# Optimization experiments

Hardware: AMD Instinct MI355X
Metric: run time of the kernel (lower is better)

Reference implementation:

```python
import jax, jax.numpy as jnp
import numpy as np

B, IN_DIM, OUT_DIM, DEGREE = 4096, 1024, 1024, 4
LN_EPS = 1e-5


def setup_inputs() -> dict:
    key = jax.random.key(0)
    k_x, k_c = jax.random.split(key)
    x = jax.random.normal(k_x, (B, IN_DIM), dtype=jnp.float32)
    # xavier_normal_ on tensor of shape (in, out, deg+1): fan_in/fan_out from
    # torch convention: fan_in = out*(deg+1)? torch computes fan_in=size(1)*receptive,
    # for 3D tensor fan_in = shape[1]*shape[2], fan_out = shape[0]*shape[2].
    fan_in = OUT_DIM * (DEGREE + 1)
    fan_out = IN_DIM * (DEGREE + 1)
    std = float(np.sqrt(2.0 / (fan_in + fan_out)))
    cheby_coeffs = jax.random.normal(k_c, (IN_DIM, OUT_DIM, DEGREE + 1), dtype=jnp.float32) * std
    ln_weight = jnp.ones((IN_DIM,), dtype=jnp.float32)
    ln_bias = jnp.zeros((IN_DIM,), dtype=jnp.float32)
    return {"x": x, "cheby_coeffs": cheby_coeffs, "ln_weight": ln_weight, "ln_bias": ln_bias}


def _layer_norm(x, w, b):
    mu = jnp.mean(x, axis=-1, keepdims=True)
    var = jnp.mean(jnp.square(x - mu), axis=-1, keepdims=True)
    return (x - mu) * jax.lax.rsqrt(var + LN_EPS) * w + b


def reference(x, cheby_coeffs, ln_weight, ln_bias):
    h = jnp.tanh(_layer_norm(x, ln_weight, ln_bias))  # [B, I]
    # Chebyshev recurrence T0=1, T1=h, T_{n}=2h*T_{n-1}-T_{n-2}
    cheby = [jnp.ones_like(h), h]
    for _ in range(2, DEGREE + 1):
        cheby.append(2.0 * h * cheby[-1] - cheby[-2])
    stacked = jnp.stack(cheby, axis=-1)  # [B, I, D+1]
    y = jnp.einsum('bid,iod->bo', stacked, cheby_coeffs)
    return jax.nn.silu(y)
```

## Files before the change

kernel.cpp:

```cpp
#include <hip/hip_runtime.h>
#include <cstdint>
#include <cstddef>

#define BATCH 4096
#define IDIM 1024
#define ODIM 1024
#define KDIM 4096
#define KHALF 2048

typedef __attribute__((ext_vector_type(8))) short bf16x8;
typedef __attribute__((ext_vector_type(4))) float f32x4;

__device__ __forceinline__ unsigned short f2bf(float f) {
  union { float f; unsigned int u; } v; v.f = f;
  unsigned int r = (v.u + 0x7FFFu + ((v.u >> 16) & 1u)) >> 16;
  return (unsigned short)r;
}
__device__ __forceinline__ float bf2f(unsigned short u) {
  union { unsigned int u; float f; } v; v.u = ((unsigned int)u) << 16;
  return v.f;
}

__device__ __forceinline__ void load_lds16(const void* g, void* l) {
  __builtin_amdgcn_global_load_lds(
      (const __attribute__((address_space(1))) void*)g,
      (__attribute__((address_space(3))) void*)l, 16, 0, 0);
}

__device__ __forceinline__ int sidx(int p, int ii) {
  return p * 64 + ((ii + 4 * (p & 15)) & 63);
}

__global__ __launch_bounds__(256) void prep(
    const float* __restrict__ x, const float* __restrict__ lnw,
    const float* __restrict__ lnb, const float* __restrict__ C,
    unsigned short* __restrict__ A, unsigned short* __restrict__ Bt,
    float* __restrict__ biasPart) {
  __shared__ __align__(16) unsigned short sm[64 * 5 * 64];
  int bid = blockIdx.x;
  int t = threadIdx.x;

  if (bid < BATCH) {
    float* rs = (float*)sm;
    float* rq = ((float*)sm) + 4;
    const float4 v = ((const float4*)(x + (size_t)bid * IDIM))[t];
    float s  = v.x + v.y + v.z + v.w;
    float s2 = v.x * v.x + v.y * v.y + v.z * v.z + v.w * v.w;
#pragma unroll
    for (int off = 32; off > 0; off >>= 1) {
      s  += __shfl_down(s, off);
      s2 += __shfl_down(s2, off);
    }
    int lane = t & 63, wv = t >> 6;
    if (lane == 0) { rs[wv] = s; rq[wv] = s2; }
    __syncthreads();
    float S1 = rs[0] + rs[1] + rs[2] + rs[3];
    float S2 = rq[0] + rq[1] + rq[2] + rq[3];
    float mean = S1 * (1.0f / IDIM);
    float var  = S2 * (1.0f / IDIM) - mean * mean;
    float rstd = rsqrtf(var + 1e-5f);

    const float4 w4 = ((const float4*)lnw)[t];
    const float4 b4 = ((const float4*)lnb)[t];
    float xs[4]  = {v.x, v.y, v.z, v.w};
    float ws4[4] = {w4.x, w4.y, w4.z, w4.w};
    float bs4[4] = {b4.x, b4.y, b4.z, b4.w};

    unsigned short u1[4], u2[4], u3[4], u4[4];
#pragma unroll
    for (int j = 0; j < 4; j++) {
      float h  = tanhf((xs[j] - mean) * rstd * ws4[j] + bs4[j]);
      float T2 = 2.0f * h * h - 1.0f;
      float T3 = 2.0f * h * T2 - h;
      float T4 = 2.0f * h * T3 - T2;
      u1[j] = f2bf(h); u2[j] = f2bf(T2); u3[j] = f2bf(T3); u4[j] = f2bf(T4);
    }
    size_t base = (size_t)bid * KDIM;
    *(ushort4*)(A + base + 0 * IDIM + t * 4) = *(ushort4*)u1;
    *(ushort4*)(A + base + 1 * IDIM + t * 4) = *(ushort4*)u2;
    *(ushort4*)(A + base + 2 * IDIM + t * 4) = *(ushort4*)u3;
    *(ushort4*)(A + base + 3 * IDIM + t * 4) = *(ushort4*)u4;
  } else {
    int cb = bid - BATCH;
    int i0 = (cb & 15) * 64, o0 = (cb >> 4) * 64;
#pragma unroll
    for (int r = 0; r < 20; r++) {
      int idx = r * 256 + t;
      int ii  = idx / 80;
      int c4  = idx - ii * 80;
      const float4 f = *(const float4*)(C + ((size_t)(i0 + ii) * ODIM + o0) * 5 + c4 * 4);
      float vals[4] = {f.x, f.y, f.z, f.w};
#pragma unroll
      for (int j = 0; j < 4; j++) {
        int p = c4 * 4 + j;
        sm[sidx(p, ii)] = f2bf(vals[j]);
      }
    }
    __syncthreads();
#pragma unroll
    for (int r = 0; r < 16; r++) {
      int idx = r * 256 + t;
      int seg = idx >> 4, l16 = idx & 15;
      int oo = seg >> 2, d2 = seg & 3;
      int p = oo * 5 + d2 + 1;
      const unsigned short* src = &sm[sidx(p, l16 * 4)];
      ushort4 u = *(const ushort4*)src;
      *(ushort4*)(Bt + (size_t)(o0 + oo) * KDIM + d2 * IDIM + i0 + l16 * 4) = u;
    }
    if (t < 64) {
      float s = 0.f;
      int p = t * 5;
#pragma unroll
      for (int ii = 0; ii < 64; ii++) s += bf2f(sm[sidx(p, ii)]);
      biasPart[(size_t)(i0 >> 6) * ODIM + o0 + t] = s;
    }
  }
}

#define BM 128
#define BN 128
#define BK 64
#define NIT (KHALF / BK)

__global__ __launch_bounds__(256, 2) void gemm_part(
    const unsigned short* __restrict__ A,
    const unsigned short* __restrict__ Bt,
    const float* __restrict__ biasPart,
    float* __restrict__ out0,
    float* __restrict__ part1) {
  __shared__ unsigned short As[2 * BM * BK];
  __shared__ unsigned short Bs[2 * BN * BK];
  int t = threadIdx.x;
  int lane = t & 63, w = t >> 6;
  int m0 = blockIdx.x * BM;
  int n0 = blockIdx.y * BN;
  size_t kbase = (size_t)blockIdx.z * KHALF;

  f32x4 acc[4][4];
#pragma unroll
  for (int i = 0; i < 4; i++)
#pragma unroll
    for (int j = 0; j < 4; j++) acc[i][j] = (f32x4){0.f, 0.f, 0.f, 0.f};

  int wm = (w >> 1) * 64;
  int wn = (w & 1) * 64;

  int sr = lane >> 3;
  int sc = ((lane & 7) ^ sr) * 8;
  const unsigned short* ag[4]; unsigned short* al[4];
  const unsigned short* bg[4]; unsigned short* bl[4];
#pragma unroll
  for (int q = 0; q < 4; q++) {
    int row = w * 8 + q * 32;
    ag[q] = A  + (size_t)(m0 + row + sr) * KDIM + kbase + sc;
    al[q] = &As[row * BK];
    bg[q] = Bt + (size_t)(n0 + row + sr) * KDIM + kbase + sc;
    bl[q] = &Bs[row * BK];
  }

  int arow = (wm + (lane & 15)) * BK;
  int brow = (wn + (lane & 15)) * BK;
  int x7 = lane & 7, hi = lane >> 4;

#define ISSUE(buf, kk0)                                                     \
  do {                                                                      \
    int _k = (kk0);                                                         \
    _Pragma("unroll")                                                       \
    for (int q = 0; q < 4; q++) load_lds16(ag[q] + _k, al[q] + (buf) * (BM * BK)); \
    _Pragma("unroll")                                                       \
    for (int q = 0; q < 4; q++) load_lds16(bg[q] + _k, bl[q] + (buf) * (BN * BK)); \
  } while (0)

#define COMPUTE(buf)                                                        \
  do {                                                                      \
    _Pragma("unroll")                                                       \
    for (int kk = 0; kk < 2; kk++) {                                        \
      int co = ((kk * 4 + hi) ^ x7) * 8;                                    \
      bf16x8 af[4], bfv[4];                                                 \
      _Pragma("unroll")                                                     \
      for (int i = 0; i < 4; i++)                                           \
        af[i]  = *(const bf16x8*)&As[(buf) * (BM * BK) + arow + i * 16 * BK + co]; \
      _Pragma("unroll")                                                     \
      for (int j = 0; j < 4; j++)                                           \
        bfv[j] = *(const bf16x8*)&Bs[(buf) * (BN * BK) + brow + j * 16 * BK + co]; \
      _Pragma("unroll")                                                     \
      for (int i = 0; i < 4; i++)                                           \
        _Pragma("unroll")                                                   \
        for (int j = 0; j < 4; j++)                                         \
          acc[i][j] = __builtin_amdgcn_mfma_f32_16x16x32_bf16(af[i], bfv[j], acc[i][j], 0, 0, 0); \
    }                                                                       \
  } while (0)

  ISSUE(0, 0);
  for (int it = 0; it < NIT; it += 2) {
    __syncthreads();
    if (it + 1 < NIT) ISSUE(1, (it + 1) * BK);
    COMPUTE(0);
    __syncthreads();
    if (it + 2 < NIT) ISSUE(0, (it + 2) * BK);
    COMPUTE(1);
  }

  float* dst = (blockIdx.z == 0) ? out0 : part1;
  bool addb = (blockIdx.z == 0);
#pragma unroll
  for (int j = 0; j < 4; j++) {
    int col = n0 + wn + j * 16 + (lane & 15);
    float bc = 0.f;
    if (addb) {
#pragma unroll
      for (int ib = 0; ib < 16; ib++) bc += biasPart[(size_t)ib * ODIM + col];
    }
#pragma unroll
    for (int i = 0; i < 4; i++) {
      int row = m0 + wm + i * 16 + hi * 4;
#pragma unroll
      for (int r = 0; r < 4; r++)
        dst[(size_t)(row + r) * ODIM + col] = acc[i][j][r] + bc;
    }
  }
}

__global__ __launch_bounds__(256) void reduce_silu(
    float* __restrict__ out, const float* __restrict__ part1) {
  int idx = blockIdx.x * 256 + threadIdx.x;
  float4 a = ((const float4*)out)[idx];
  float4 b = ((const float4*)part1)[idx];
  float y0 = a.x + b.x, y1 = a.y + b.y, y2 = a.z + b.z, y3 = a.w + b.w;
  float4 o;
  o.x = y0 / (1.0f + __expf(-y0));
  o.y = y1 / (1.0f + __expf(-y1));
  o.z = y2 / (1.0f + __expf(-y2));
  o.w = y3 / (1.0f + __expf(-y3));
  ((float4*)out)[idx] = o;
}

extern "C" void kernel_launch(void* const* d_in, const int* in_sizes, int n_in,
                              void* d_out, int out_size, void* d_ws, size_t ws_size,
                              hipStream_t stream) {
  const float* x    = (const float*)d_in[0];
  const float* coef = (const float*)d_in[1];
  const float* lnw  = (const float*)d_in[2];
  const float* lnb  = (const float*)d_in[3];
  float* out = (float*)d_out;

  char* ws = (char*)d_ws;
  unsigned short* A  = (unsigned short*)ws;
  unsigned short* Bt = (unsigned short*)(ws + (size_t)BATCH * KDIM * 2);
  char* p = ws + (size_t)BATCH * KDIM * 2 + (size_t)ODIM * KDIM * 2;
  float* biasPart = (float*)p;
  float* part1 = (float*)(p + 16 * ODIM * sizeof(float));

  prep<<<BATCH + 256, 256, 0, stream>>>(x, lnw, lnb, coef, A, Bt, biasPart);
  gemm_part<<<dim3(BATCH / BM, ODIM / BN, 2), 256, 0, stream>>>(A, Bt, biasPart, out, part1);
  reduce_silu<<<(BATCH * ODIM) / (256 * 4), 256, 0, stream>>>(out, part1);
}
```

Measured before the change: 138.4 us.

## Split GEMM K dimension four ways with smaller K tiles and higher occupancy

Raises split-K from 2 to 4 partitions and halves the K tile from 64 to 32. The LDS swizzle and load mapping are reworked for the narrower tile, and launch bounds now allow 4 blocks per CU. The grid grows from 512 to 1024 blocks to improve CU fill and latency hiding. The cost is writing and re-reading three full fp32 partial buffers in the reduce kernel instead of one, plus more barrier syncs per unit of MFMA work.

```diff
diff --git a/kernel.cpp b/kernel.cpp
--- a/kernel.cpp
+++ b/kernel.cpp
@@ -6,7 +6,7 @@
 #define IDIM 1024
 #define ODIM 1024
 #define KDIM 4096
-#define KHALF 2048
+#define KQ   1024
 
 typedef __attribute__((ext_vector_type(8))) short bf16x8;
 typedef __attribute__((ext_vector_type(4))) float f32x4;
@@ -119,22 +119,22 @@
 
 #define BM 128
 #define BN 128
-#define BK 64
-#define NIT (KHALF / BK)
-
-__global__ __launch_bounds__(256, 2) void gemm_part(
+#define BK 32
+#define NIT (KQ / BK)
+
+__global__ __launch_bounds__(256, 4) void gemm_part(
     const unsigned short* __restrict__ A,
     const unsigned short* __restrict__ Bt,
     const float* __restrict__ biasPart,
     float* __restrict__ out0,
-    float* __restrict__ part1) {
+    float* __restrict__ parts) {
   __shared__ unsigned short As[2 * BM * BK];
   __shared__ unsigned short Bs[2 * BN * BK];
   int t = threadIdx.x;
   int lane = t & 63, w = t >> 6;
   int m0 = blockIdx.x * BM;
   int n0 = blockIdx.y * BN;
-  size_t kbase = (size_t)blockIdx.z * KHALF;
+  size_t kbase = (size_t)blockIdx.z * KQ;
 
   f32x4 acc[4][4];
 #pragma unroll
@@ -145,50 +145,48 @@
   int wm = (w >> 1) * 64;
   int wn = (w & 1) * 64;
 
-  int sr = lane >> 3;
-  int sc = ((lane & 7) ^ sr) * 8;
-  const unsigned short* ag[4]; unsigned short* al[4];
-  const unsigned short* bg[4]; unsigned short* bl[4];
-#pragma unroll
-  for (int q = 0; q < 4; q++) {
-    int row = w * 8 + q * 32;
-    ag[q] = A  + (size_t)(m0 + row + sr) * KDIM + kbase + sc;
+  int lr  = lane >> 2;
+  int kcs = ((lane & 3) - (lr >> 1)) & 3;
+  int sco = kcs * 8;
+  const unsigned short* ag[2]; unsigned short* al[2];
+  const unsigned short* bg[2]; unsigned short* bl[2];
+#pragma unroll
+  for (int q = 0; q < 2; q++) {
+    int row = w * 32 + q * 16;
+    ag[q] = A  + (size_t)(m0 + row + lr) * KDIM + kbase + sco;
     al[q] = &As[row * BK];
-    bg[q] = Bt + (size_t)(n0 + row + sr) * KDIM + kbase + sc;
+    bg[q] = Bt + (size_t)(n0 + row + lr) * KDIM + kbase + sco;
     bl[q] = &Bs[row * BK];
   }
 
-  int arow = (wm + (lane & 15)) * BK;
-  int brow = (wn + (lane & 15)) * BK;
-  int x7 = lane & 7, hi = lane >> 4;
+  int l15 = lane & 15, hi = lane >> 4;
+  int co = ((hi + (l15 >> 1)) & 3) * 8;
+  int arow = (wm + l15) * BK + co;
+  int brow = (wn + l15) * BK + co;
 
 #define ISSUE(buf, kk0)                                                     \
   do {                                                                      \
     int _k = (kk0);                                                         \
     _Pragma("unroll")                                                       \
-    for (int q = 0; q < 4; q++) load_lds16(ag[q] + _k, al[q] + (buf) * (BM * BK)); \
-    _Pragma("unroll")                                                       \
-    for (int q = 0; q < 4; q++) load_lds16(bg[q] + _k, bl[q] + (buf) * (BN * BK)); \
+    for (int q = 0; q < 2; q++) load_lds16(ag[q] + _k, al[q] + (buf) * (BM * BK)); \
+    _Pragma("unroll")                                                       \
+    for (int q = 0; q < 2; q++) load_lds16(bg[q] + _k, bl[q] + (buf) * (BN * BK)); \
   } while (0)
 
 #define COMPUTE(buf)                                                        \
   do {                                                                      \
-    _Pragma("unroll")                                                       \
-    for (int kk = 0; kk < 2; kk++) {                                        \
-      int co = ((kk * 4 + hi) ^ x7) * 8;                                    \
-      bf16x8 af[4], bfv[4];                                                 \
-      _Pragma("unroll")                                                     \
-      for (int i = 0; i < 4; i++)                                           \
-        af[i]  = *(const bf16x8*)&As[(buf) * (BM * BK) + arow + i * 16 * BK + co]; \
+    bf16x8 af[4], bfv[4];                                                   \
+    _Pragma("unroll")                                                       \
+    for (int i = 0; i < 4; i++)                                             \
+      af[i]  = *(const bf16x8*)&As[(buf) * (BM * BK) + arow + i * 16 * BK]; \
+    _Pragma("unroll")                                                       \
+    for (int j = 0; j < 4; j++)                                             \
+      bfv[j] = *(const bf16x8*)&Bs[(buf) * (BN * BK) + brow + j * 16 * BK]; \
+    _Pragma("unroll")                                                       \
+    for (int i = 0; i < 4; i++)                                             \
       _Pragma("unroll")                                                     \
       for (int j = 0; j < 4; j++)                                           \
-        bfv[j] = *(const bf16x8*)&Bs[(buf) * (BN * BK) + brow + j * 16 * BK + co]; \
-      _Pragma("unroll")                                                     \
-      for (int i = 0; i < 4; i++)                                           \
-        _Pragma("unroll")                                                   \
-        for (int j = 0; j < 4; j++)                                         \
-          acc[i][j] = __builtin_amdgcn_mfma_f32_16x16x32_bf16(af[i], bfv[j], acc[i][j], 0, 0, 0); \
-    }                                                                       \
+        acc[i][j] = __builtin_amdgcn_mfma_f32_16x16x32_bf16(af[i], bfv[j], acc[i][j], 0, 0, 0); \
   } while (0)
 
   ISSUE(0, 0);
@@ -201,11 +199,12 @@
     COMPUTE(1);
   }
 
-  float* dst = (blockIdx.z == 0) ? out0 : part1;
-  bool addb = (blockIdx.z == 0);
+  int z = blockIdx.z;
+  float* dst = (z == 0) ? out0 : (parts + (size_t)(z - 1) * BATCH * ODIM);
+  bool addb = (z == 0);
 #pragma unroll
   for (int j = 0; j < 4; j++) {
-    int col = n0 + wn + j * 16 + (lane & 15);
+    int col = n0 + wn + j * 16 + l15;
     float bc = 0.f;
     if (addb) {
 #pragma unroll
@@ -222,11 +221,17 @@
 }
 
 __global__ __launch_bounds__(256) void reduce_silu(
-    float* __restrict__ out, const float* __restrict__ part1) {
+    float* __restrict__ out, const float* __restrict__ parts) {
   int idx = blockIdx.x * 256 + threadIdx.x;
-  float4 a = ((const float4*)out)[idx];
-  float4 b = ((const float4*)part1)[idx];
-  float y0 = a.x + b.x, y1 = a.y + b.y, y2 = a.z + b.z, y3 = a.w + b.w;
+  const size_t SZ4 = (size_t)BATCH * ODIM / 4;
+  float4 a  = ((const float4*)out)[idx];
+  float4 p0 = ((const float4*)parts)[idx];
+  float4 p1 = ((const float4*)parts)[idx + SZ4];
+  float4 p2 = ((const float4*)parts)[idx + 2 * SZ4];
+  float y0 = a.x + p0.x + p1.x + p2.x;
+  float y1 = a.y + p0.y + p1.y + p2.y;
+  float y2 = a.z + p0.z + p1.z + p2.z;
+  float y3 = a.w + p0.w + p1.w + p2.w;
   float4 o;
   o.x = y0 / (1.0f + __expf(-y0));
   o.y = y1 / (1.0f + __expf(-y1));
@@ -249,9 +254,9 @@
   unsigned short* Bt = (unsigned short*)(ws + (size_t)BATCH * KDIM * 2);
   char* p = ws + (size_t)BATCH * KDIM * 2 + (size_t)ODIM * KDIM * 2;
   float* biasPart = (float*)p;
-  float* part1 = (float*)(p + 16 * ODIM * sizeof(float));
+  float* parts = (float*)(p + 16 * ODIM * sizeof(float));
 
   prep<<<BATCH + 256, 256, 0, stream>>>(x, lnw, lnb, coef, A, Bt, biasPart);
-  gemm_part<<<dim3(BATCH / BM, ODIM / BN, 2), 256, 0, stream>>>(A, Bt, biasPart, out, part1);
-  reduce_silu<<<(BATCH * ODIM) / (256 * 4), 256, 0, stream>>>(out, part1);
-}
+  gemm_part<<<dim3(BATCH / BM, ODIM / BN, 4), 256, 0, stream>>>(A, Bt, biasPart, out, parts);
+  reduce_silu<<<(BATCH * ODIM) / (256 * 4), 256, 0, stream>>>(out, parts);
+}
```

Measured after the change: 157.4 us. 13.7% more time.
